# Optimization experiments

Measured on AMD Instinct MI355X. Metric: run time of the kernel, lower is better.

## Reference

```python
import jax, jax.numpy as jnp
import numpy as np
import math


def _build_coeffs(max_l):
    """Replicates RSHxyz._init_coefficients with exact integer/half-integer math.
    Returns (dst_pointers[T], clm_tuvs[T], xpows[T], ypows[T], zpows[T], ns_lms[(max_l+1)^2]).
    """
    dst, clm, px, py, pz, ns = [], [], [], [], [], []
    for l in range(max_l + 1):
        for m in range(-l, l + 1):
            am = abs(m)
            # ns_lm = 1/(2^|m| l!) * sqrt(2 (l+|m|)! (l-|m|)! / 2^(m==0))
            ns.append(
                1.0 / (2 ** am * math.factorial(l))
                * math.sqrt(2.0 * math.factorial(l + am) * math.factorial(l - am)
                            / (2.0 if m == 0 else 1.0))
            )
            # v is half-integer when m<0; track v2 = 2*v as an int
            v2_start = 1 if m < 0 else 0  # vm(m) = 0.5*(m<0), v starts at vm
            v2_stop = 2 * ((am - 1) // 2 if m < 0 else am // 2) + v2_start  # inclusive
            for t in range((l - am) // 2 + 1):
                for u in range(t + 1):
                    for v2 in range(v2_start, v2_stop + 1, 2):
                        parity = (t + (v2 - v2_start) // 2) % 2  # t + v - vm(m)
                        c = ((-1.0 if parity else 1.0)
                             * 0.25 ** t
                             * math.comb(l, t)
                             * (math.comb(l - t, am + t) if am + t <= l - t else 0)
                             * math.comb(t, u)
                             * (math.comb(am, v2) if v2 <= am else 0))
                        dst.append(l * (l + 1) + m)
                        clm.append(c)
                        px.append(2 * t + am - 2 * u - v2)
                        py.append(2 * u + v2)
                        pz.append(l - 2 * t - am)
    return (np.asarray(dst, np.int32), np.asarray(clm, np.float32),
            np.asarray(px, np.int32), np.asarray(py, np.int32),
            np.asarray(pz, np.int32), np.asarray(ns, np.float32))


def setup_inputs() -> dict:
    max_l = 6
    N = 500_000
    dst, clm, px, py, pz, ns = _build_coeffs(max_l)
    key = jax.random.key(0)
    xyz = jax.random.normal(key, (N, 3), dtype=jnp.float32)
    return {
        "xyz": xyz,
        "clm_tuvs": jnp.asarray(clm),
        "ns_lms": jnp.asarray(ns),
        "dst_pointers": jnp.asarray(dst),
        "xpows": jnp.asarray(px),
        "ypows": jnp.asarray(py),
        "zpows": jnp.asarray(pz),
        "max_l": max_l,
    }


def _pow_table(x, max_pow):
    # [N] -> [N, max_pow+1] with col k = x**k, built by repeated multiply so
    # negative bases and 0**0==1 are handled exactly (matches torch masked pow).
    cols = [jnp.ones_like(x)]
    for _ in range(max_pow):
        cols.append(cols[-1] * x)
    return jnp.stack(cols, axis=-1)


def reference(xyz, clm_tuvs, ns_lms, dst_pointers, xpows, ypows, zpows, max_l):
    xyz = xyz.reshape(-1, 3)
    tx = _pow_table(xyz[:, 0], max_l)  # [N, max_l+1]
    ty = _pow_table(xyz[:, 1], max_l)
    tz = _pow_table(xyz[:, 2], max_l)
    # monomials x^px * y^py * z^pz scaled by C^{lm}_{tuv}: [N, T]
    poly = tx[:, xpows] * ty[:, ypows] * tz[:, zpows] * clm_tuvs
    n_out = ns_lms.shape[0]  # (max_l+1)^2
    out = jnp.zeros((poly.shape[0], n_out), poly.dtype).at[:, dst_pointers].add(poly)
    return out * ns_lms
```

## Files before the change

### kernel.cpp

```cpp
#include <hip/hip_runtime.h>


namespace {

constexpr int MAXL   = 6;
constexpr int NOUT   = (MAXL + 1) * (MAXL + 1);
constexpr int NT_MAX = 256;

struct Tab {
    int   dst[NT_MAX];
    int   px[NT_MAX];
    int   py[NT_MAX];
    int   pz[NT_MAX];
    float clm[NT_MAX];
    int   cnt;
};

constexpr long long comb(int n, int k) {
    if (k < 0 || k > n) return 0;
    long long r = 1;
    for (int i = 0; i < k; ++i) r = r * (n - i) / (i + 1);
    return r;
}

constexpr Tab build_tab() {
    Tab tb{};
    int k = 0;
    for (int l = 0; l <= MAXL; ++l) {
        for (int m = -l; m <= l; ++m) {
            const int am  = (m < 0) ? -m : m;
            const int v2s = (m < 0) ? 1 : 0;
            const int v2e = 2 * ((m < 0) ? (am - 1) / 2 : am / 2) + v2s;
            for (int t = 0; t <= (l - am) / 2; ++t) {
                for (int u = 0; u <= t; ++u) {
                    for (int v2 = v2s; v2 <= v2e; v2 += 2) {
                        const int parity = (t + (v2 - v2s) / 2) % 2;
                        double c = parity ? -1.0 : 1.0;
                        for (int i = 0; i < t; ++i) c *= 0.25;
                        c *= (double)comb(l, t);
                        c *= (double)((am + t <= l - t) ? comb(l - t, am + t) : 0);
                        c *= (double)comb(t, u);
                        c *= (double)((v2 <= am) ? comb(am, v2) : 0);
                        tb.dst[k] = l * (l + 1) + m;
                        tb.px[k]  = 2 * t + am - 2 * u - v2;
                        tb.py[k]  = 2 * u + v2;
                        tb.pz[k]  = l - 2 * t - am;
                        tb.clm[k] = (float)c;
                        ++k;
                    }
                }
            }
        }
    }
    tb.cnt = k;
    return tb;
}

constexpr Tab TB = build_tab();
static_assert(TB.cnt == 188, "expected 188 terms for max_l=6");

constexpr int BLOCK = 256;

}

__global__ __launch_bounds__(BLOCK) void rsh_kernel(const float* __restrict__ xyz,
                                                    const float* __restrict__ ns,
                                                    float* __restrict__ out,
                                                    int N) {
    __shared__ float sm[BLOCK * NOUT];

    const int tid = threadIdx.x;
    const long long i = (long long)blockIdx.x * BLOCK + tid;

    float x = 0.f, y = 0.f, z = 0.f;
    if (i < N) {
        const float* p = xyz + i * 3;
        x = p[0]; y = p[1]; z = p[2];
    }

    float xp[MAXL + 1], yp[MAXL + 1], zp[MAXL + 1];
    xp[0] = yp[0] = zp[0] = 1.f;
#pragma unroll
    for (int p = 1; p <= MAXL; ++p) {
        xp[p] = xp[p - 1] * x;
        yp[p] = yp[p - 1] * y;
        zp[p] = zp[p - 1] * z;
    }

    float acc[NOUT];
#pragma unroll
    for (int o = 0; o < NOUT; ++o) acc[o] = 0.f;

#pragma unroll
    for (int k = 0; k < TB.cnt; ++k) {
        const float mono = xp[TB.px[k]] * yp[TB.py[k]] * zp[TB.pz[k]];
        acc[TB.dst[k]] = fmaf(TB.clm[k], mono, acc[TB.dst[k]]);
    }

#pragma unroll
    for (int o = 0; o < NOUT; ++o) sm[tid * NOUT + o] = acc[o] * ns[o];

    __syncthreads();

    const float4* sm4 = (const float4*)sm;
    float4* out4 = (float4*)out;
    const long long base4 = (long long)blockIdx.x * (BLOCK * NOUT / 4);
    const long long lim4 = (long long)N * NOUT / 4;
#pragma unroll 1
    for (int idx = tid; idx < BLOCK * NOUT / 4; idx += BLOCK) {
        const long long g = base4 + idx;
        if (g < lim4) out4[g] = sm4[idx];
    }
}

extern "C" void kernel_launch(void* const* d_in, const int* in_sizes, int n_in,
                              void* d_out, int out_size, void* d_ws, size_t ws_size,
                              hipStream_t stream) {
    const float* xyz = (const float*)d_in[0];
    const float* ns  = (const float*)d_in[2];
    float* out = (float*)d_out;

    const int N = in_sizes[0] / 3;
    const int grid = (N + BLOCK - 1) / BLOCK;
    rsh_kernel<<<grid, BLOCK, 0, stream>>>(xyz, ns, out, N);
}
```

Measured before the change: 118.4 us.

## Halve LDS staging with two-phase compute/store, vectorized input loads, nontemporal stores

Loads xyz coalesced as float4 through shared memory, then computes outputs in two halves of 128 threads each. This cuts shared memory from 256x49 floats to 128x49, which should raise occupancy. Each half writes its slab with nontemporal float4 stores. A single running accumulator with per-(l,m) flush replaces the 49-register accumulator array to lower register pressure. The trade-off is that only half the block computes at a time, with extra barriers serializing compute and store.

```diff
diff --git a/kernel.cpp b/kernel.cpp
--- a/kernel.cpp
+++ b/kernel.cpp
@@ -7,12 +7,15 @@
 constexpr int NOUT   = (MAXL + 1) * (MAXL + 1);
 constexpr int NT_MAX = 256;
 
+typedef float f4 __attribute__((ext_vector_type(4)));
+
 struct Tab {
     int   dst[NT_MAX];
     int   px[NT_MAX];
     int   py[NT_MAX];
     int   pz[NT_MAX];
     float clm[NT_MAX];
+    bool  last[NT_MAX];
     int   cnt;
 };
 
@@ -46,10 +49,12 @@
                         tb.py[k]  = 2 * u + v2;
                         tb.pz[k]  = l - 2 * t - am;
                         tb.clm[k] = (float)c;
+                        tb.last[k] = false;
                         ++k;
                     }
                 }
             }
+            tb.last[k - 1] = true;
         }
     }
     tb.cnt = k;
@@ -60,6 +65,8 @@
 static_assert(TB.cnt == 188, "expected 188 terms for max_l=6");
 
 constexpr int BLOCK = 256;
+constexpr int HALF  = 128;
+constexpr int SLAB4 = HALF * NOUT / 4;
 
 }
 
@@ -67,50 +74,87 @@
                                                     const float* __restrict__ ns,
                                                     float* __restrict__ out,
                                                     int N) {
-    __shared__ float sm[BLOCK * NOUT];
+    __shared__ float sm[HALF * NOUT];
 
     const int tid = threadIdx.x;
-    const long long i = (long long)blockIdx.x * BLOCK + tid;
+    const int blk = blockIdx.x;
 
-    float x = 0.f, y = 0.f, z = 0.f;
-    if (i < N) {
-        const float* p = xyz + i * 3;
-        x = p[0]; y = p[1]; z = p[2];
+    {
+        const int nf = N * 3;
+        const int g0 = blk * (BLOCK * 3 / 4);
+        if (tid < BLOCK * 3 / 4) {
+            const f4* x4 = (const f4*)xyz;
+            f4 v = (f4){0.f, 0.f, 0.f, 0.f};
+            const int g = g0 + tid;
+            if (g * 4 + 3 < nf) {
+                v = x4[g];
+            } else {
+#pragma unroll
+                for (int t = 0; t < 4; ++t) {
+                    const int f = g * 4 + t;
+                    if (f < nf) v[t] = xyz[f];
+                }
+            }
+            ((f4*)sm)[tid] = v;
+        }
     }
-
-    float xp[MAXL + 1], yp[MAXL + 1], zp[MAXL + 1];
-    xp[0] = yp[0] = zp[0] = 1.f;
-#pragma unroll
-    for (int p = 1; p <= MAXL; ++p) {
-        xp[p] = xp[p - 1] * x;
-        yp[p] = yp[p - 1] * y;
-        zp[p] = zp[p - 1] * z;
-    }
-
-    float acc[NOUT];
-#pragma unroll
-    for (int o = 0; o < NOUT; ++o) acc[o] = 0.f;
-
-#pragma unroll
-    for (int k = 0; k < TB.cnt; ++k) {
-        const float mono = xp[TB.px[k]] * yp[TB.py[k]] * zp[TB.pz[k]];
-        acc[TB.dst[k]] = fmaf(TB.clm[k], mono, acc[TB.dst[k]]);
-    }
-
-#pragma unroll
-    for (int o = 0; o < NOUT; ++o) sm[tid * NOUT + o] = acc[o] * ns[o];
-
     __syncthreads();
 
-    const float4* sm4 = (const float4*)sm;
-    float4* out4 = (float4*)out;
-    const long long base4 = (long long)blockIdx.x * (BLOCK * NOUT / 4);
-    const long long lim4 = (long long)N * NOUT / 4;
-#pragma unroll 1
-    for (int idx = tid; idx < BLOCK * NOUT / 4; idx += BLOCK) {
-        const long long g = base4 + idx;
-        if (g < lim4) out4[g] = sm4[idx];
-    }
+    const float x = sm[tid * 3 + 0];
+    const float y = sm[tid * 3 + 1];
+    const float z = sm[tid * 3 + 2];
+    __syncthreads();
+
+    const int lim4 = (N * NOUT) >> 2;
+    const int remF = (N * NOUT) & 3;
+
+    auto compute_and_stage = [&](int r) {
+        float xp[MAXL + 1], yp[MAXL + 1], zp[MAXL + 1];
+        xp[0] = yp[0] = zp[0] = 1.f;
+#pragma unroll
+        for (int p = 1; p <= MAXL; ++p) {
+            xp[p] = xp[p - 1] * x;
+            yp[p] = yp[p - 1] * y;
+            zp[p] = zp[p - 1] * z;
+        }
+        float acc = 0.f;
+#pragma unroll
+        for (int k = 0; k < TB.cnt; ++k) {
+            acc = fmaf(TB.clm[k], xp[TB.px[k]] * yp[TB.py[k]] * zp[TB.pz[k]], acc);
+            if (TB.last[k]) {
+                sm[r * NOUT + TB.dst[k]] = acc * ns[TB.dst[k]];
+                acc = 0.f;
+            }
+        }
+    };
+
+    auto store_slab = [&](int phase) {
+        const f4* s4 = (const f4*)sm;
+        f4* o4 = (f4*)out;
+        const int base4 = blk * (BLOCK * NOUT / 4) + phase * SLAB4;
+#pragma unroll
+        for (int it = 0; it < (SLAB4 + BLOCK - 1) / BLOCK; ++it) {
+            const int f = it * BLOCK + tid;
+            if (f < SLAB4) {
+                const int g = base4 + f;
+                if (g < lim4) {
+                    __builtin_nontemporal_store(s4[f], o4 + g);
+                } else if (g == lim4 && remF) {
+#pragma unroll
+                    for (int t = 0; t < 3; ++t)
+                        if (t < remF) out[g * 4 + t] = sm[f * 4 + t];
+                }
+            }
+        }
+    };
+
+    if (tid < HALF) compute_and_stage(tid);
+    __syncthreads();
+    store_slab(0);
+    __syncthreads();
+    if (tid >= HALF) compute_and_stage(tid - HALF);
+    __syncthreads();
+    store_slab(1);
 }
 
 extern "C" void kernel_launch(void* const* d_in, const int* in_sizes, int n_in,
```

Measured after the change: 123.2 us. 4.1% more time.
